# Performance work log

Measured on AMD Instinct MI355X. Metric: run time of the kernel, lower is better.

The kernel has to match this reference:

```python
import jax, jax.numpy as jnp
import numpy as np

IN_DIM = 5
T = 1.0
MU, NU, SIGMA = 0.1, 0.2, 0.3
BN_EPS = 1e-5
FLOOR = 1e-4


def _linear_init(key, fan_in, fan_out):
    kw, kb = jax.random.split(key)
    bound = 1.0 / np.sqrt(fan_in)
    w = jax.random.uniform(kw, (fan_in, fan_out), minval=-bound, maxval=bound, dtype=jnp.float32)
    b = jax.random.uniform(kb, (fan_out,), minval=-bound, maxval=bound, dtype=jnp.float32)
    return w, b


def setup_inputs() -> dict:
    key = jax.random.key(0)
    ks = jax.random.split(key, 12)
    B, N, D = 8192, 100, 1
    indim = IN_DIM + 4  # bn(typeVec) + (t, X) + mx + mc
    w1, b1 = _linear_init(ks[0], indim, 64)
    w2, b2 = _linear_init(ks[1], 64, 64)
    w3, b3 = _linear_init(ks[2], 64, 1)
    wc1, bc1 = _linear_init(ks[3], indim, 64)
    wc2, bc2 = _linear_init(ks[4], 64, 64)
    wc3, bc3 = _linear_init(ks[5], 64, 1)
    return {
        'bm': jax.random.normal(ks[6], (B, N, D), dtype=jnp.float32),
        'cn': jax.random.normal(ks[7], (B, N + 1, D), dtype=jnp.float32),
        'typeVec': jax.random.uniform(ks[8], (B, IN_DIM), dtype=jnp.float32),
        'mx': jax.random.uniform(ks[9], (B, N + 1, D), dtype=jnp.float32),
        'mc': jax.random.uniform(ks[10], (B, N, D), dtype=jnp.float32),
        'initial': jnp.ones((1,), dtype=jnp.float32),
        'bn_gamma': jnp.ones((IN_DIM,), dtype=jnp.float32),
        'bn_beta': jnp.zeros((IN_DIM,), dtype=jnp.float32),
        'bnc_gamma': jnp.ones((IN_DIM,), dtype=jnp.float32),
        'bnc_beta': jnp.zeros((IN_DIM,), dtype=jnp.float32),
        'w1': w1, 'b1': b1, 'w2': w2, 'b2': b2, 'w3': w3, 'b3': b3,
        'wc1': wc1, 'bc1': bc1, 'wc2': wc2, 'bc2': bc2, 'wc3': wc3, 'bc3': bc3,
    }


def _batchnorm(x, gamma, beta):
    # training-mode BatchNorm1d: batch stats, biased variance
    m = x.mean(axis=0)
    v = ((x - m) ** 2).mean(axis=0)
    return (x - m) * jax.lax.rsqrt(v + BN_EPS) * gamma + beta


def _mlp(feat, w1, b1, w2, b2, w3, b3):
    h = jax.nn.relu(feat @ w1 + b1)
    h = jax.nn.relu(h @ w2 + b2)
    return h @ w3 + b3


def reference(bm, cn, typeVec, mx, mc, initial,
              bn_gamma, bn_beta, bnc_gamma, bnc_beta,
              w1, b1, w2, b2, w3, b3,
              wc1, bc1, wc2, bc2, wc3, bc3):
    B, N, D = bm.shape
    dt = T / N
    # bn(typeVec) is identical at every step (same batch), compute once
    bn_out = _batchnorm(typeVec, bn_gamma, bn_beta)    # (B, in_dim)
    bnc_out = _batchnorm(typeVec, bnc_gamma, bnc_beta)  # (B, in_dim)
    dcn = cn[:, 1:] - cn[:, :-1]                        # (B, N, 1)
    t_prev = (jnp.arange(N) * dt).astype(bm.dtype)      # t_{i-1} for i=1..N

    def step(x, inp):
        bm_i, dcn_i, mx_i, mc_i, tp = inp               # (B,1) each; tp scalar
        t_col = jnp.full((x.shape[0], 1), tp, dtype=x.dtype)
        feat_pi = jnp.concatenate([bn_out, t_col, x, mx_i, mc_i], axis=1)
        feat_c = jnp.concatenate([bnc_out, t_col, x, mx_i, mc_i], axis=1)
        pi = _mlp(feat_pi, w1, b1, w2, b2, w3, b3)      # (B,1)
        c = jnp.exp(_mlp(feat_c, wc1, bc1, wc2, bc2, wc3, bc3))  # (B,1)
        # invest-consumption wealth SDE one-step (mode.one_step_simulation)
        x_new = x + pi * x * (MU * dt + NU * bm_i + SIGMA * dcn_i) - c * x * dt
        x_new = jax.nn.relu(x_new - FLOOR) + FLOOR
        return x_new, x_new

    x0 = jnp.broadcast_to(initial.astype(bm.dtype), (B, 1))
    xs = (jnp.moveaxis(bm, 1, 0), jnp.moveaxis(dcn, 1, 0),
          jnp.moveaxis(mx[:, :N], 1, 0), jnp.moveaxis(mc, 1, 0), t_prev)
    _, states = jax.lax.scan(step, x0, xs)              # (N, B, 1)
    states = jnp.concatenate([x0[None], states], axis=0)  # (N+1, B, 1)
    states = jnp.moveaxis(states, 0, 1)                 # (B, N+1, 1)
    times = jnp.broadcast_to((jnp.arange(N + 1) * dt).astype(bm.dtype)[None, :, None], (B, N + 1, 1))
    return jnp.concatenate([times, states], axis=2)     # (B, N+1, 2)
```

## Files before the change

### kernel.cpp

```cpp
#include <hip/hip_runtime.h>
#include <math.h>

#define IN_DIM 5
constexpr int B = 8192;
constexpr int N = 100;
constexpr float DT     = 0.01f;
constexpr float MU_DT  = 0.001f;
constexpr float NU     = 0.2f;
constexpr float SIGMA  = 0.3f;
constexpr float BN_EPS = 1e-5f;
constexpr float FLOORV = 1e-4f;

typedef __attribute__((ext_vector_type(8))) short short8;
typedef __attribute__((ext_vector_type(4))) float f32x4;
typedef __attribute__((ext_vector_type(2))) float f32x2;
typedef __attribute__((ext_vector_type(4))) int   i32x4;

__device__ __forceinline__ void bf16_split(float h, short& hi, short& lo) {
    unsigned int ub = __builtin_bit_cast(unsigned int, h);
    hi = (short)(ub >> 16);
    float hif = __builtin_bit_cast(float, ub & 0xffff0000u);
    float l = h - hif;
    lo = (short)(__builtin_bit_cast(unsigned int, l) >> 16);
}

__device__ __forceinline__ float red16(float v) {
#if __has_builtin(__builtin_amdgcn_update_dpp)
    int x;
    x = __builtin_amdgcn_update_dpp(0, __builtin_bit_cast(int, v), 0xB1, 0xF, 0xF, false);
    v += __builtin_bit_cast(float, x);
    x = __builtin_amdgcn_update_dpp(0, __builtin_bit_cast(int, v), 0x4E, 0xF, 0xF, false);
    v += __builtin_bit_cast(float, x);
    x = __builtin_amdgcn_update_dpp(0, __builtin_bit_cast(int, v), 0x141, 0xF, 0xF, false);
    v += __builtin_bit_cast(float, x);
    x = __builtin_amdgcn_update_dpp(0, __builtin_bit_cast(int, v), 0x140, 0xF, 0xF, false);
    v += __builtin_bit_cast(float, x);
    return v;
#else
    v += __shfl_xor(v, 1);
    v += __shfl_xor(v, 2);
    v += __shfl_xor(v, 4);
    v += __shfl_xor(v, 8);
    return v;
#endif
}

#define KEEPV(v) asm volatile("" : "+v"(v))
#define KEEPS8(v) { f32x4 _kt = __builtin_bit_cast(f32x4, v); asm volatile("" : "+v"(_kt)); \
                    v = __builtin_bit_cast(short8, _kt); }

__global__ __launch_bounds__(1024) void bn_stats_kernel(
    const float* __restrict__ tv,
    const float* __restrict__ g1, const float* __restrict__ be1,
    const float* __restrict__ g2, const float* __restrict__ be2,
    float* __restrict__ ws)
{
    const int t = threadIdx.x;
    float s[IN_DIM] = {0.f, 0.f, 0.f, 0.f, 0.f};
    float q[IN_DIM] = {0.f, 0.f, 0.f, 0.f, 0.f};
    for (int r = t; r < B; r += 1024) {
        const float* row = tv + r * IN_DIM;
#pragma unroll
        for (int k = 0; k < IN_DIM; ++k) {
            const float v = row[k];
            s[k] += v;
            q[k] += v * v;
        }
    }
#pragma unroll
    for (int k = 0; k < IN_DIM; ++k) {
#pragma unroll
        for (int off = 32; off >= 1; off >>= 1) {
            s[k] += __shfl_xor(s[k], off);
            q[k] += __shfl_xor(q[k], off);
        }
    }
    __shared__ float red[16][2 * IN_DIM];
    const int w = t >> 6, lane = t & 63;
    if (lane == 0) {
#pragma unroll
        for (int k = 0; k < IN_DIM; ++k) {
            red[w][k] = s[k];
            red[w][IN_DIM + k] = q[k];
        }
    }
    __syncthreads();
    if (t == 0) {
#pragma unroll
        for (int k = 0; k < IN_DIM; ++k) {
            float S = 0.f, Q = 0.f;
            for (int u = 0; u < 16; ++u) { S += red[u][k]; Q += red[u][IN_DIM + k]; }
            const float mean = S / (float)B;
            const float var  = Q / (float)B - mean * mean;
            const float inv  = 1.0f / sqrtf(var + BN_EPS);
            const float a1 = inv * g1[k];
            const float a2 = inv * g2[k];
            ws[k]          = a1;
            ws[IN_DIM + k] = be1[k] - mean * a1;
            ws[10 + k]     = a2;
            ws[15 + k]     = be2[k] - mean * a2;
        }
    }
}

__global__ __launch_bounds__(256, 2) void sim_kernel(
    const float* __restrict__ bm, const float* __restrict__ cn,
    const float* __restrict__ typeVec,
    const float* __restrict__ mx, const float* __restrict__ mc,
    const float* __restrict__ initial,
    const float* __restrict__ w1, const float* __restrict__ b1,
    const float* __restrict__ w2, const float* __restrict__ b2,
    const float* __restrict__ w3, const float* __restrict__ b3,
    const float* __restrict__ wc1, const float* __restrict__ bc1,
    const float* __restrict__ wc2, const float* __restrict__ bc2,
    const float* __restrict__ wc3, const float* __restrict__ bc3,
    const float* __restrict__ ws, float* __restrict__ out)
{
    const int tid = threadIdx.x;
    const int wid = tid >> 6;
    const int l   = tid & 63;
    const int s   = l & 15;
    const int g   = l >> 4;
    const int mlp = wid & 1;
    const int q   = wid >> 1;
    const int b0  = blockIdx.x * 16;

    __shared__ float4 SI[N][16];
    __shared__ float  traj[N + 1][16];
    __shared__ float4 ex[16];
    __shared__ short8 FX[2][2][2][64];

#pragma unroll
    for (int k = 0; k < 8; ++k) {
        const int f  = tid + 256 * k;
        const int ss = f >> 7;
        const int ii = f & 127;
        if (ii < N) {
            const size_t r = (size_t)(b0 + ss);
            const float vb = bm[r * N + ii];
            const float c0 = cn[r * (N + 1) + ii];
            const float c1 = cn[r * (N + 1) + ii + 1];
            const float vx = mx[r * (N + 1) + ii];
            const float vc = mc[r * N + ii];
            SI[ii][ss] = make_float4(vb, c1 - c0, vx, vc);
        }
    }

    const float* W1 = mlp ? wc1 : w1;
    const float* B1 = mlp ? bc1 : b1;
    const float* W2 = mlp ? wc2 : w2;
    const float* B2 = mlp ? bc2 : b2;
    const float* W3 = mlp ? wc3 : w3;
    const float* B3 = mlp ? bc3 : b3;
    const float* alpha = ws + (mlp ? 10 : 0);
    const float* beta  = ws + (mlp ? 15 : 5);

    short8 BhO[2], BlO[2], BhX[2], BlX[2];
#pragma unroll
    for (int ntl = 0; ntl < 2; ++ntl) {
        const int nt = 2 * q + ntl;
        short8 fhO, flO, fhX, flX;
#pragma unroll
        for (int e = 0; e < 8; ++e) {
            short hi, lo;
            bf16_split(W2[(32 * q + 8 * g + e) * 64 + 16 * nt + s], hi, lo);
            fhO[e] = hi; flO[e] = lo;
            bf16_split(W2[(32 * (1 - q) + 8 * g + e) * 64 + 16 * nt + s], hi, lo);
            fhX[e] = hi; flX[e] = lo;
        }
        BhO[ntl] = fhO; BlO[ntl] = flO;
        BhX[ntl] = fhX; BlX[ntl] = flX;
    }

    float bnv[IN_DIM];
    {
        const float* tvp = typeVec + (size_t)(b0 + s) * IN_DIM;
#pragma unroll
        for (int k = 0; k < IN_DIM; ++k)
            bnv[k] = fmaf(tvp[k], alpha[k], beta[k]);
    }
    f32x2 bs2[4], wt2[4], wx2[4], wm2[4], wr2[4];
#pragma unroll
    for (int p = 0; p < 4; ++p) {
#pragma unroll
        for (int c = 0; c < 2; ++c) {
            const int j = 2 * p + c;
            const int u = 32 * q + 8 * g + j;
            wt2[p][c] = W1[5 * 64 + u];
            wx2[p][c] = W1[6 * 64 + u];
            wm2[p][c] = W1[7 * 64 + u];
            wr2[p][c] = W1[8 * 64 + u];
            float a = B1[u];
#pragma unroll
            for (int k = 0; k < IN_DIM; ++k) a = fmaf(bnv[k], W1[k * 64 + u], a);
            bs2[p][c] = a;
        }
    }
    f32x2 b2v, w3v;
#pragma unroll
    for (int ntl = 0; ntl < 2; ++ntl) {
        const int nt = 2 * q + ntl;
        b2v[ntl] = B2[16 * nt + s];
        w3v[ntl] = W3[16 * nt + s];
    }
    float b3s = B3[0];
    const float x0 = initial[0];

#pragma unroll
    for (int ntl = 0; ntl < 2; ++ntl) {
        KEEPS8(BhO[ntl]); KEEPS8(BlO[ntl]); KEEPS8(BhX[ntl]); KEEPS8(BlX[ntl]);
    }
#pragma unroll
    for (int p = 0; p < 4; ++p) {
        KEEPV(bs2[p]); KEEPV(wt2[p]); KEEPV(wx2[p]); KEEPV(wm2[p]); KEEPV(wr2[p]);
    }
    KEEPV(b2v); KEEPV(w3v); KEEPV(b3s);

    float x = x0;
    if (tid < 16) traj[0][tid] = x0;
    __syncthreads();

    float4 in_cur = SI[0][s];

    for (int i = 0; i < N; ++i) {
        const float t = (float)i * DT;
        const float4 in = in_cur;
        if (i + 1 < N) in_cur = SI[i + 1][s];

        const f32x2 t2  = {t, t};
        const f32x2 x2  = {x, x};
        const f32x2 mx2 = {in.z, in.z};
        const f32x2 mc2 = {in.w, in.w};
        const f32x2 z2  = {0.f, 0.f};
        unsigned int hp[4], lp[4];
#pragma unroll
        for (int p = 0; p < 4; ++p) {
            f32x2 h = __builtin_elementwise_fma(wt2[p], t2, bs2[p]);
            h = __builtin_elementwise_fma(wx2[p], x2, h);
            h = __builtin_elementwise_fma(wm2[p], mx2, h);
            h = __builtin_elementwise_fma(wr2[p], mc2, h);
            h = __builtin_elementwise_max(h, z2);
            const unsigned int u0 = __builtin_bit_cast(unsigned int, h[0]);
            const unsigned int u1 = __builtin_bit_cast(unsigned int, h[1]);
            hp[p] = (u0 >> 16) | (u1 & 0xffff0000u);
            const float t0 = __builtin_bit_cast(float, u0 & 0xffff0000u);
            const float t1 = __builtin_bit_cast(float, u1 & 0xffff0000u);
            const float r0f = h[0] - t0;
            const float r1f = h[1] - t1;
            lp[p] = (__builtin_bit_cast(unsigned int, r0f) >> 16) |
                    (__builtin_bit_cast(unsigned int, r1f) & 0xffff0000u);
        }
        const short8 oh = __builtin_bit_cast(short8, (i32x4){(int)hp[0], (int)hp[1], (int)hp[2], (int)hp[3]});
        const short8 ol = __builtin_bit_cast(short8, (i32x4){(int)lp[0], (int)lp[1], (int)lp[2], (int)lp[3]});

        FX[mlp][q][0][l] = oh;
        FX[mlp][q][1][l] = ol;
        __syncthreads();
        const short8 xh = FX[mlp][1 - q][0][l];
        const short8 xl = FX[mlp][1 - q][1][l];

        f32x4 acc0[2], acc1[2];
#pragma unroll
        for (int ntl = 0; ntl < 2; ++ntl) {
            acc0[ntl] = (f32x4){b2v[ntl], b2v[ntl], b2v[ntl], b2v[ntl]};
            acc1[ntl] = (f32x4){0.f, 0.f, 0.f, 0.f};
        }
#pragma unroll
        for (int ntl = 0; ntl < 2; ++ntl) {
            acc0[ntl] = __builtin_amdgcn_mfma_f32_16x16x32_bf16(oh, BhO[ntl], acc0[ntl], 0, 0, 0);
            acc0[ntl] = __builtin_amdgcn_mfma_f32_16x16x32_bf16(ol, BhO[ntl], acc0[ntl], 0, 0, 0);
            acc0[ntl] = __builtin_amdgcn_mfma_f32_16x16x32_bf16(oh, BlO[ntl], acc0[ntl], 0, 0, 0);
            acc1[ntl] = __builtin_amdgcn_mfma_f32_16x16x32_bf16(xh, BhX[ntl], acc1[ntl], 0, 0, 0);
            acc1[ntl] = __builtin_amdgcn_mfma_f32_16x16x32_bf16(xl, BhX[ntl], acc1[ntl], 0, 0, 0);
            acc1[ntl] = __builtin_amdgcn_mfma_f32_16x16x32_bf16(xh, BlX[ntl], acc1[ntl], 0, 0, 0);
        }

        f32x4 rv = (f32x4){0.f, 0.f, 0.f, 0.f};
        const f32x4 z4 = (f32x4){0.f, 0.f, 0.f, 0.f};
#pragma unroll
        for (int ntl = 0; ntl < 2; ++ntl) {
            const f32x4 fs  = acc0[ntl] + acc1[ntl];
            const f32x4 rel = __builtin_elementwise_max(fs, z4);
            const f32x4 wsp = (f32x4){w3v[ntl], w3v[ntl], w3v[ntl], w3v[ntl]};
            rv = __builtin_elementwise_fma(rel, wsp, rv);
        }
        const float r0 = red16(rv[0]);
        const float r1 = red16(rv[1]);
        const float r2 = red16(rv[2]);
        const float r3 = red16(rv[3]);

        const int r4 = l & 15;
        float wv = r0;
        wv = (r4 == 1) ? r1 : wv;
        wv = (r4 == 2) ? r2 : wv;
        wv = (r4 == 3) ? r3 : wv;
        if (q == 0) wv += b3s;
        if (r4 < 4) ((float*)&ex[4 * g + r4])[wid] = wv;
        __syncthreads();

        const float4 pv = ex[s];
        const float pi_v = pv.x + pv.z;
        const float c_v  = __expf(pv.y + pv.w);
        const float drift = MU_DT + fmaf(NU, in.x, SIGMA * in.y);
        float xn = x + pi_v * x * drift - c_v * x * DT;
        xn = fmaxf(xn - FLOORV, 0.0f) + FLOORV;
        x = xn;

        if (tid < 16) traj[i + 1][tid] = x;
    }
    __syncthreads();

    const int TOT = 16 * (N + 1) * 2;
#pragma unroll
    for (int k = 0; k < 13; ++k) {
        const int e = tid + 256 * k;
        if (e < TOT) {
            const int sample = e / (2 * (N + 1));
            const int r      = e - sample * (2 * (N + 1));
            const int i      = r >> 1;
            const float v    = (r & 1) ? traj[i][sample] : (float)i * DT;
            out[(size_t)b0 * (2 * (N + 1)) + e] = v;
        }
    }
}

extern "C" void kernel_launch(void* const* d_in, const int* in_sizes, int n_in,
                              void* d_out, int out_size, void* d_ws, size_t ws_size,
                              hipStream_t stream) {
    const float* bm        = (const float*)d_in[0];
    const float* cn        = (const float*)d_in[1];
    const float* typeVec   = (const float*)d_in[2];
    const float* mx        = (const float*)d_in[3];
    const float* mc        = (const float*)d_in[4];
    const float* initial   = (const float*)d_in[5];
    const float* bn_gamma  = (const float*)d_in[6];
    const float* bn_beta   = (const float*)d_in[7];
    const float* bnc_gamma = (const float*)d_in[8];
    const float* bnc_beta  = (const float*)d_in[9];
    const float* w1  = (const float*)d_in[10];
    const float* b1  = (const float*)d_in[11];
    const float* w2  = (const float*)d_in[12];
    const float* b2  = (const float*)d_in[13];
    const float* w3  = (const float*)d_in[14];
    const float* b3  = (const float*)d_in[15];
    const float* wc1 = (const float*)d_in[16];
    const float* bc1 = (const float*)d_in[17];
    const float* wc2 = (const float*)d_in[18];
    const float* bc2 = (const float*)d_in[19];
    const float* wc3 = (const float*)d_in[20];
    const float* bc3 = (const float*)d_in[21];
    float* wsp = (float*)d_ws;
    float* out = (float*)d_out;

    bn_stats_kernel<<<1, 1024, 0, stream>>>(typeVec, bn_gamma, bn_beta,
                                            bnc_gamma, bnc_beta, wsp);
    sim_kernel<<<512, 256, 0, stream>>>(bm, cn, typeVec, mx, mc, initial,
                                        w1, b1, w2, b2, w3, b3,
                                        wc1, bc1, wc2, bc2, wc3, bc3,
                                        wsp, out);
}
```

Before: 86.16 us.

## Compute full hidden layer per wave to drop per-step LDS exchange barrier

Each wave now computes all 64 first-layer hidden units itself instead of half, so the shared-memory exchange of the other half and its __syncthreads per step are removed. The exchange buffer for the final reduction is double-buffered by step parity, which lets one barrier per iteration suffice. In exchange, the first-layer FMA work per wave doubles and more weights stay resident in registers. A waves_per_eu(2,2) attribute is added to keep occupancy fixed at two waves per EU.

```diff
diff --git a/kernel.cpp b/kernel.cpp
--- a/kernel.cpp
+++ b/kernel.cpp
@@ -103,7 +103,9 @@
     }
 }
 
-__global__ __launch_bounds__(256, 2) void sim_kernel(
+__global__ __launch_bounds__(256, 2)
+__attribute__((amdgpu_waves_per_eu(2, 2)))
+void sim_kernel(
     const float* __restrict__ bm, const float* __restrict__ cn,
     const float* __restrict__ typeVec,
     const float* __restrict__ mx, const float* __restrict__ mc,
@@ -116,19 +118,18 @@
     const float* __restrict__ wc3, const float* __restrict__ bc3,
     const float* __restrict__ ws, float* __restrict__ out)
 {
-    const int tid = threadIdx.x;
-    const int wid = tid >> 6;
-    const int l   = tid & 63;
-    const int s   = l & 15;
-    const int g   = l >> 4;
-    const int mlp = wid & 1;
-    const int q   = wid >> 1;
-    const int b0  = blockIdx.x * 16;
+    const int tid  = threadIdx.x;
+    const int wid  = tid >> 6;
+    const int l    = tid & 63;
+    const int s    = l & 15;
+    const int g    = l >> 4;
+    const int mlp  = wid & 1;
+    const int half = wid >> 1;
+    const int b0   = blockIdx.x * 16;
 
     __shared__ float4 SI[N][16];
     __shared__ float  traj[N + 1][16];
-    __shared__ float4 ex[16];
-    __shared__ short8 FX[2][2][2][64];
+    __shared__ float4 ex[2][16];
 
 #pragma unroll
     for (int k = 0; k < 8; ++k) {
@@ -155,21 +156,21 @@
     const float* alpha = ws + (mlp ? 10 : 0);
     const float* beta  = ws + (mlp ? 15 : 5);
 
-    short8 BhO[2], BlO[2], BhX[2], BlX[2];
-#pragma unroll
-    for (int ntl = 0; ntl < 2; ++ntl) {
-        const int nt = 2 * q + ntl;
-        short8 fhO, flO, fhX, flX;
-#pragma unroll
-        for (int e = 0; e < 8; ++e) {
-            short hi, lo;
-            bf16_split(W2[(32 * q + 8 * g + e) * 64 + 16 * nt + s], hi, lo);
-            fhO[e] = hi; flO[e] = lo;
-            bf16_split(W2[(32 * (1 - q) + 8 * g + e) * 64 + 16 * nt + s], hi, lo);
-            fhX[e] = hi; flX[e] = lo;
-        }
-        BhO[ntl] = fhO; BlO[ntl] = flO;
-        BhX[ntl] = fhX; BlX[ntl] = flX;
+    short8 Bh[2][2], Bl[2][2];
+#pragma unroll
+    for (int kt = 0; kt < 2; ++kt) {
+#pragma unroll
+        for (int ntl = 0; ntl < 2; ++ntl) {
+            const int nt = 2 * half + ntl;
+            short8 fh, fl;
+#pragma unroll
+            for (int e = 0; e < 8; ++e) {
+                short hi, lo;
+                bf16_split(W2[(32 * kt + 8 * g + e) * 64 + 16 * nt + s], hi, lo);
+                fh[e] = hi; fl[e] = lo;
+            }
+            Bh[kt][ntl] = fh; Bl[kt][ntl] = fl;
+        }
     }
 
     float bnv[IN_DIM];
@@ -179,13 +180,13 @@
         for (int k = 0; k < IN_DIM; ++k)
             bnv[k] = fmaf(tvp[k], alpha[k], beta[k]);
     }
-    f32x2 bs2[4], wt2[4], wx2[4], wm2[4], wr2[4];
-#pragma unroll
-    for (int p = 0; p < 4; ++p) {
+    f32x2 bs2[8], wt2[8], wx2[8], wm2[8], wr2[8];
+#pragma unroll
+    for (int p = 0; p < 8; ++p) {
 #pragma unroll
         for (int c = 0; c < 2; ++c) {
             const int j = 2 * p + c;
-            const int u = 32 * q + 8 * g + j;
+            const int u = (j < 8) ? (8 * g + j) : (32 + 8 * g + (j - 8));
             wt2[p][c] = W1[5 * 64 + u];
             wx2[p][c] = W1[6 * 64 + u];
             wm2[p][c] = W1[7 * 64 + u];
@@ -199,7 +200,7 @@
     f32x2 b2v, w3v;
 #pragma unroll
     for (int ntl = 0; ntl < 2; ++ntl) {
-        const int nt = 2 * q + ntl;
+        const int nt = 2 * half + ntl;
         b2v[ntl] = B2[16 * nt + s];
         w3v[ntl] = W3[16 * nt + s];
     }
@@ -207,11 +208,11 @@
     const float x0 = initial[0];
 
 #pragma unroll
-    for (int ntl = 0; ntl < 2; ++ntl) {
-        KEEPS8(BhO[ntl]); KEEPS8(BlO[ntl]); KEEPS8(BhX[ntl]); KEEPS8(BlX[ntl]);
-    }
-#pragma unroll
-    for (int p = 0; p < 4; ++p) {
+    for (int kt = 0; kt < 2; ++kt)
+#pragma unroll
+        for (int ntl = 0; ntl < 2; ++ntl) { KEEPS8(Bh[kt][ntl]); KEEPS8(Bl[kt][ntl]); }
+#pragma unroll
+    for (int p = 0; p < 8; ++p) {
         KEEPV(bs2[p]); KEEPV(wt2[p]); KEEPV(wx2[p]); KEEPV(wm2[p]); KEEPV(wr2[p]);
     }
     KEEPV(b2v); KEEPV(w3v); KEEPV(b3s);
@@ -232,9 +233,9 @@
         const f32x2 mx2 = {in.z, in.z};
         const f32x2 mc2 = {in.w, in.w};
         const f32x2 z2  = {0.f, 0.f};
-        unsigned int hp[4], lp[4];
-#pragma unroll
-        for (int p = 0; p < 4; ++p) {
+        unsigned int hp[8], lp[8];
+#pragma unroll
+        for (int p = 0; p < 8; ++p) {
             f32x2 h = __builtin_elementwise_fma(wt2[p], t2, bs2[p]);
             h = __builtin_elementwise_fma(wx2[p], x2, h);
             h = __builtin_elementwise_fma(wm2[p], mx2, h);
@@ -250,14 +251,10 @@
             lp[p] = (__builtin_bit_cast(unsigned int, r0f) >> 16) |
                     (__builtin_bit_cast(unsigned int, r1f) & 0xffff0000u);
         }
-        const short8 oh = __builtin_bit_cast(short8, (i32x4){(int)hp[0], (int)hp[1], (int)hp[2], (int)hp[3]});
-        const short8 ol = __builtin_bit_cast(short8, (i32x4){(int)lp[0], (int)lp[1], (int)lp[2], (int)lp[3]});
-
-        FX[mlp][q][0][l] = oh;
-        FX[mlp][q][1][l] = ol;
-        __syncthreads();
-        const short8 xh = FX[mlp][1 - q][0][l];
-        const short8 xl = FX[mlp][1 - q][1][l];
+        const short8 ah0 = __builtin_bit_cast(short8, (i32x4){(int)hp[0], (int)hp[1], (int)hp[2], (int)hp[3]});
+        const short8 ah1 = __builtin_bit_cast(short8, (i32x4){(int)hp[4], (int)hp[5], (int)hp[6], (int)hp[7]});
+        const short8 al0 = __builtin_bit_cast(short8, (i32x4){(int)lp[0], (int)lp[1], (int)lp[2], (int)lp[3]});
+        const short8 al1 = __builtin_bit_cast(short8, (i32x4){(int)lp[4], (int)lp[5], (int)lp[6], (int)lp[7]});
 
         f32x4 acc0[2], acc1[2];
 #pragma unroll
@@ -267,12 +264,12 @@
         }
 #pragma unroll
         for (int ntl = 0; ntl < 2; ++ntl) {
-            acc0[ntl] = __builtin_amdgcn_mfma_f32_16x16x32_bf16(oh, BhO[ntl], acc0[ntl], 0, 0, 0);
-            acc0[ntl] = __builtin_amdgcn_mfma_f32_16x16x32_bf16(ol, BhO[ntl], acc0[ntl], 0, 0, 0);
-            acc0[ntl] = __builtin_amdgcn_mfma_f32_16x16x32_bf16(oh, BlO[ntl], acc0[ntl], 0, 0, 0);
-            acc1[ntl] = __builtin_amdgcn_mfma_f32_16x16x32_bf16(xh, BhX[ntl], acc1[ntl], 0, 0, 0);
-            acc1[ntl] = __builtin_amdgcn_mfma_f32_16x16x32_bf16(xl, BhX[ntl], acc1[ntl], 0, 0, 0);
-            acc1[ntl] = __builtin_amdgcn_mfma_f32_16x16x32_bf16(xh, BlX[ntl], acc1[ntl], 0, 0, 0);
+            acc0[ntl] = __builtin_amdgcn_mfma_f32_16x16x32_bf16(ah0, Bh[0][ntl], acc0[ntl], 0, 0, 0);
+            acc0[ntl] = __builtin_amdgcn_mfma_f32_16x16x32_bf16(al0, Bh[0][ntl], acc0[ntl], 0, 0, 0);
+            acc0[ntl] = __builtin_amdgcn_mfma_f32_16x16x32_bf16(ah0, Bl[0][ntl], acc0[ntl], 0, 0, 0);
+            acc1[ntl] = __builtin_amdgcn_mfma_f32_16x16x32_bf16(ah1, Bh[1][ntl], acc1[ntl], 0, 0, 0);
+            acc1[ntl] = __builtin_amdgcn_mfma_f32_16x16x32_bf16(al1, Bh[1][ntl], acc1[ntl], 0, 0, 0);
+            acc1[ntl] = __builtin_amdgcn_mfma_f32_16x16x32_bf16(ah1, Bl[1][ntl], acc1[ntl], 0, 0, 0);
         }
 
         f32x4 rv = (f32x4){0.f, 0.f, 0.f, 0.f};
@@ -294,11 +291,11 @@
         wv = (r4 == 1) ? r1 : wv;
         wv = (r4 == 2) ? r2 : wv;
         wv = (r4 == 3) ? r3 : wv;
-        if (q == 0) wv += b3s;
-        if (r4 < 4) ((float*)&ex[4 * g + r4])[wid] = wv;
+        if (half == 0) wv += b3s;
+        if (r4 < 4) ((float*)&ex[i & 1][4 * g + r4])[wid] = wv;
         __syncthreads();
 
-        const float4 pv = ex[s];
+        const float4 pv = ex[i & 1][s];
         const float pi_v = pv.x + pv.z;
         const float c_v  = __expf(pv.y + pv.w);
         const float drift = MU_DT + fmaf(NU, in.x, SIGMA * in.y);
```

New measurement: 97.57 us. 13.2% more time.
